# Optimization experiments

Hardware: AMD Instinct MI355X
Metric: run time of the kernel (lower is better)

## Reference

```python
import jax, jax.numpy as jnp
import numpy as np

M = 2          # n_mix
D_K = 128      # feature dim
TEMP = float(np.sqrt(D_K))  # temperature = d_k ** 0.5


def setup_inputs() -> dict:
    key = jax.random.key(0)
    k1, k2, k3, k4 = jax.random.split(key, 4)
    BS, N, N2 = 8, 2048, 2048
    qt = jax.random.normal(k1, (BS, N, D_K), jnp.float32)
    kt = jax.random.normal(k2, (BS, N2, D_K), jnp.float32)
    vt = jax.random.normal(k3, (BS, N2, D_K), jnp.float32)
    std = M ** -0.5
    kernel = jax.random.uniform(k4, (M, D_K), jnp.float32, -std, std)
    return {"qt": qt, "kt": kt, "vt": vt, "kernel": kernel}


def reference(qt, kt, vt, kernel):
    # channels_last path of MixtureOfSoftMaxACF.call, training=False (dropout = identity)
    BS, N, dk = qt.shape
    N2 = kt.shape[1]
    d = dk // M
    # mixture prior: softmax(kernel @ mean_q^T) over axis=1 (faithful to Softmax(axis=1))
    bar_qt = jnp.mean(qt, axis=1)                       # (BS, dk)
    prior_mix = jax.nn.softmax(kernel @ bar_qt.T, axis=1)  # (m, BS)
    prior_mix = prior_mix.reshape(BS * M, 1, 1)            # row-major reshape, as in TF
    # split features into mixtures via row-major reshape (as tf.reshape does)
    q = qt.reshape(BS * M, N, d)
    k = kt.reshape(BS * M, N2, d)
    att = jnp.einsum('bnd,bmd->bnm', q, k) / TEMP        # (BS*m, N, N2)
    att = jax.nn.softmax(att, axis=2)
    att = (att * prior_mix).reshape(BS, M, N, N2).sum(axis=1)  # (BS, N, N2)
    return att @ vt                                      # (BS, N, d_v)
```

## Files before the change

kernel.cpp:

```cpp
#include <hip/hip_runtime.h>
#include <hip/hip_fp16.h>

typedef float    f32x4 __attribute__((ext_vector_type(4)));
typedef _Float16 f16x2 __attribute__((ext_vector_type(2)));
typedef _Float16 f16x4 __attribute__((ext_vector_type(4)));
typedef _Float16 f16x8 __attribute__((ext_vector_type(8)));

#define BS 8
#define NN 2048
#define DK 128
#define DM 64
#define MIXOFF (1024 * DK)
#define QSCALE 0.12751744116926208f

#define MFMA32(a, b, c) __builtin_amdgcn_mfma_f32_16x16x32_f16((a), (b), (c), 0, 0, 0)
#define EXP2(x) __builtin_amdgcn_exp2f(x)

__device__ __forceinline__ f16x2 pkrtz(float x, float y) {
  return __builtin_bit_cast(f16x2, __builtin_amdgcn_cvt_pkrtz(x, y));
}

__device__ __forceinline__ void load_lds16(const _Float16* g, _Float16* l) {
  __builtin_amdgcn_global_load_lds(
      (const __attribute__((address_space(1))) void*)(uintptr_t)g,
      (__attribute__((address_space(3))) void*)(uint32_t)(uintptr_t)l, 16, 0, 0);
}

__global__ void prep_k(const float* __restrict__ kt, _Float16* __restrict__ kh,
                       const float* __restrict__ vt, _Float16* __restrict__ vT,
                       const float* __restrict__ qt, float* __restrict__ qpart) {
  __shared__ float tile[64][65];
  __shared__ float red[256];
  int blk = blockIdx.x;
  int t = threadIdx.x;
  if (blk < 512) {
    size_t base = (size_t)blk * 4096;
#pragma unroll
    for (int j = 0; j < 4; ++j) {
      size_t i = base + j * 1024 + t * 4;
      f32x4 v = *(const f32x4*)(kt + i);
      f16x4 h;
      h[0] = (_Float16)v[0]; h[1] = (_Float16)v[1];
      h[2] = (_Float16)v[2]; h[3] = (_Float16)v[3];
      *(f16x4*)(kh + i) = h;
    }
  } else if (blk < 1024) {
    int i2 = blk - 512;
    int b = i2 >> 6;
    int rem = i2 & 63;
    int j0 = (rem & 31) * 64;
    int c0 = (rem >> 5) * 64;
    int tx = t & 63, ty = t >> 6;
    const float* src = vt + ((size_t)b * NN + j0) * DK + c0;
#pragma unroll
    for (int rr = 0; rr < 16; ++rr) {
      int row = ty * 16 + rr;
      tile[row][tx] = src[(size_t)row * DK + tx];
    }
    __syncthreads();
    _Float16* dst = vT + ((size_t)b * DK + c0) * NN + j0;
    int chl = t >> 4;
    int k4 = (t & 15) * 4;
#pragma unroll
    for (int r2 = 0; r2 < 4; ++r2) {
      int ch = r2 * 16 + chl;
      f16x4 h;
      h[0] = (_Float16)tile[k4 + 0][ch]; h[1] = (_Float16)tile[k4 + 1][ch];
      h[2] = (_Float16)tile[k4 + 2][ch]; h[3] = (_Float16)tile[k4 + 3][ch];
      *(f16x4*)(dst + (size_t)ch * NN + k4) = h;
    }
  } else {
    int i = blk - 1024;
    int b = i >> 3, seg = i & 7;
    int c = t & 127, h = t >> 7;
    const float* p = qt + ((size_t)b * NN + seg * 256 + h * 128) * DK + c;
    float s = 0.f;
#pragma unroll 8
    for (int n = 0; n < 128; ++n) s += p[(size_t)n * DK];
    red[t] = s;
    __syncthreads();
    if (t < 128) qpart[(size_t)i * 128 + t] = red[t] + red[t + 128];
  }
}

#define STAGE(BUF, S) do {                                                \
    _Float16* db_ = stg + (BUF) * 16384;                                  \
    load_lds16(khg + gKst + (S) * 2048, db_ + t * 8);                     \
    load_lds16(vTg + gVst + (S) * 32, db_ + 4096 + t * 8);                \
    load_lds16(khg + gKst + 65536 + (S) * 2048, db_ + 8192 + t * 8);      \
    load_lds16(vTg + gVst + 1024 + (S) * 32, db_ + 12288 + t * 8);        \
  } while (0)

__global__ __launch_bounds__(512, 2) void attn_k(const float* __restrict__ qt,
                                                 const _Float16* __restrict__ khg,
                                                 const _Float16* __restrict__ vTg,
                                                 const float* __restrict__ kern,
                                                 const float* __restrict__ qpart,
                                                 float* __restrict__ out) {
  __shared__ __align__(16) char smem[65536];
  _Float16* stg = (_Float16*)smem;
  const int b = blockIdx.x & 7;
  const int qb = blockIdx.x >> 3;
  const int t = threadIdx.x;
  const int wv = t >> 6;
  const int m = wv >> 2;
  const int kh = (wv >> 1) & 1;
  const int u = wv & 1;
  const int lane = t & 63;
  const int quad = lane >> 4, l16 = lane & 15;
  const int perm = ((l16 >> 2) << 3) | (l16 & 3);
  const int bq = b * (NN * DK);
  const int bV = b * (DK * NN);

  f16x8 qf[2][2];
#pragma unroll
  for (int su = 0; su < 2; ++su)
#pragma unroll
    for (int c = 0; c < 2; ++c) {
      const float* qp_ = qt + bq + m * MIXOFF +
                         (qb * 64 + u * 32 + su * 16 + l16) * DM + quad * 8 + c * 32;
      f32x4 v0 = *(const f32x4*)qp_;
      f32x4 v1 = *(const f32x4*)(qp_ + 4);
      union { f16x8 v; f16x2 h[4]; } w;
      w.h[0] = pkrtz(v0[0] * QSCALE, v0[1] * QSCALE);
      w.h[1] = pkrtz(v0[2] * QSCALE, v0[3] * QSCALE);
      w.h[2] = pkrtz(v1[0] * QSCALE, v1[1] * QSCALE);
      w.h[3] = pkrtz(v1[2] * QSCALE, v1[3] * QSCALE);
      qf[su][c] = w.v;
    }

  const int mixu = t >> 8;
  const int qq8 = t & 255;
  const int rK = qq8 >> 3;
  const int uuK = (qq8 & 7) ^ ((rK & 3) ^ ((rK >> 3) << 1));
  const int chV = t >> 2;
  const int uuV = (t & 3) ^ ((chV + (chV >> 2)) & 3);
  const int gKst = bq + mixu * MIXOFF + rK * 64 + uuK * 8;
  const int gVst = bV + chV * NN + uuV * 8;

  const int gK = (l16 & 3) ^ ((l16 >> 2) << 1);
  const int hV = (l16 + (l16 >> 2)) & 3;
  const int kA = (quad ^ gK) * 8;
  const int kB = ((quad + 4) ^ gK) * 8;
  const int kr0 = m * 2048 + perm * 64;
  const int kr1 = m * 2048 + (perm + 4) * 64;
  const int vbase = 4096 + l16 * 32 + (quad ^ hV) * 8;
  const int khoff = kh * 8192;

  const f32x4 z = {0.f, 0.f, 0.f, 0.f};
  f32x4 acc[2][8];
  float lsum[2] = {0.f, 0.f};
#pragma unroll
  for (int su = 0; su < 2; ++su)
#pragma unroll
    for (int cc = 0; cc < 8; ++cc) acc[su][cc] = z;

  STAGE(0, 0);
  int buf = 0;
  for (int s = 0; s < 32; ++s) {
    __syncthreads();
    if (s + 1 < 32) STAGE(buf ^ 1, s + 1);
    const _Float16* sb_ = stg + buf * 16384 + khoff;
    f16x8 kf0 = *(const f16x8*)(sb_ + kr0 + kA);
    f16x8 kf1 = *(const f16x8*)(sb_ + kr0 + kB);
    f16x8 kf2 = *(const f16x8*)(sb_ + kr1 + kA);
    f16x8 kf3 = *(const f16x8*)(sb_ + kr1 + kB);
    f16x8 vf[8];
#pragma unroll
    for (int cc = 0; cc < 8; ++cc) vf[cc] = *(const f16x8*)(sb_ + vbase + cc * 512);
#pragma unroll
    for (int su = 0; su < 2; ++su) {
      f32x4 s0 = MFMA32(kf1, qf[su][1], MFMA32(kf0, qf[su][0], z));
      f32x4 s1 = MFMA32(kf3, qf[su][1], MFMA32(kf2, qf[su][0], z));
      float e0 = EXP2(s0[0]), e1 = EXP2(s0[1]), e2 = EXP2(s0[2]), e3 = EXP2(s0[3]);
      float e4 = EXP2(s1[0]), e5 = EXP2(s1[1]), e6 = EXP2(s1[2]), e7 = EXP2(s1[3]);
      lsum[su] += ((e0 + e1) + (e2 + e3)) + ((e4 + e5) + (e6 + e7));
      union { f16x8 v; f16x2 h[4]; } w;
      w.h[0] = pkrtz(e0, e1); w.h[1] = pkrtz(e2, e3);
      w.h[2] = pkrtz(e4, e5); w.h[3] = pkrtz(e6, e7);
#pragma unroll
      for (int cc = 0; cc < 8; ++cc) acc[su][cc] = MFMA32(vf[cc], w.v, acc[su][cc]);
    }
    buf ^= 1;
  }
  __syncthreads();

  float* obuf = (float*)smem;
  float* barL = (float*)(smem + 33792);
  float* lgp = (float*)(smem + 37888);
  float* exq = (float*)(smem + 37952);
  float* prp = (float*)(smem + 38016);
  float* lbuf = (float*)(smem + 38144);

#pragma unroll
  for (int su = 0; su < 2; ++su) {
    lsum[su] += __shfl_xor(lsum[su], 16);
    lsum[su] += __shfl_xor(lsum[su], 32);
  }
  for (int e = t; e < 1024; e += 512) {
    int bb = e >> 7, c = e & 127;
    float ss = 0.f;
#pragma unroll
    for (int seg = 0; seg < 8; ++seg) ss += qpart[(size_t)(bb * 8 + seg) * 128 + c];
    barL[e] = ss * (1.0f / 2048.0f);
  }
  if (kh == 0 && quad == 0)
#pragma unroll
    for (int su = 0; su < 2; ++su) lbuf[m * 64 + u * 32 + su * 16 + l16] = lsum[su];
  __syncthreads();
  if (kh == 1 && quad == 0)
#pragma unroll
    for (int su = 0; su < 2; ++su) lbuf[m * 64 + u * 32 + su * 16 + l16] += lsum[su];
  if (t < 16) {
    int mm = t >> 3, bb = t & 7;
    float ss = 0.f;
    for (int c = 0; c < DK; ++c) ss += kern[mm * DK + c] * barL[bb * 128 + c];
    lgp[t] = ss;
  }
  __syncthreads();
  if (t < 16) {
    int mm = t >> 3;
    float mx = lgp[mm * 8];
    for (int i = 1; i < 8; ++i) mx = fmaxf(mx, lgp[mm * 8 + i]);
    exq[t] = __expf(lgp[t] - mx);
  }
  __syncthreads();
  if (t < 16) {
    int mm = t >> 3;
    float sm = 0.f;
    for (int i = 0; i < 8; ++i) sm += exq[mm * 8 + i];
    prp[t] = exq[t] / sm;
  }
  __syncthreads();

  const float wm = prp[b * 2 + m];
  float rr[2];
#pragma unroll
  for (int su = 0; su < 2; ++su)
    rr[su] = wm / lbuf[m * 64 + u * 32 + su * 16 + l16];

  if (m == 0 && kh == 0) {
#pragma unroll
    for (int su = 0; su < 2; ++su) {
      int r_ = (u * 32 + su * 16 + l16) * 132 + quad * 4;
#pragma unroll
      for (int cc = 0; cc < 8; ++cc) *(f32x4*)&obuf[r_ + cc * 16] = acc[su][cc];
    }
  }
  __syncthreads();
  if (m == 0 && kh == 1) {
#pragma unroll
    for (int su = 0; su < 2; ++su) {
      int r_ = (u * 32 + su * 16 + l16) * 132 + quad * 4;
#pragma unroll
      for (int cc = 0; cc < 8; ++cc) {
        f32x4 o = *(const f32x4*)&obuf[r_ + cc * 16];
#pragma unroll
        for (int e = 0; e < 4; ++e) o[e] = (o[e] + acc[su][cc][e]) * rr[su];
        *(f32x4*)&obuf[r_ + cc * 16] = o;
      }
    }
  }
  __syncthreads();
  if (m == 1 && kh == 0) {
#pragma unroll
    for (int su = 0; su < 2; ++su) {
      int r_ = (u * 32 + su * 16 + l16) * 132 + quad * 4;
#pragma unroll
      for (int cc = 0; cc < 8; ++cc) {
        f32x4 o = *(const f32x4*)&obuf[r_ + cc * 16];
#pragma unroll
        for (int e = 0; e < 4; ++e) o[e] += acc[su][cc][e] * rr[su];
        *(f32x4*)&obuf[r_ + cc * 16] = o;
      }
    }
  }
  __syncthreads();
  if (m == 1 && kh == 1) {
#pragma unroll
    for (int su = 0; su < 2; ++su) {
      int r_ = (u * 32 + su * 16 + l16) * 132 + quad * 4;
#pragma unroll
      for (int cc = 0; cc < 8; ++cc) {
        f32x4 o = *(const f32x4*)&obuf[r_ + cc * 16];
#pragma unroll
        for (int e = 0; e < 4; ++e) o[e] += acc[su][cc][e] * rr[su];
        *(f32x4*)&obuf[r_ + cc * 16] = o;
      }
    }
  }
  __syncthreads();
  const int row = t >> 3;
  const int cb = (t & 7) * 16;
  float* op = out + ((size_t)b * NN + qb * 64 + row) * DK + cb;
#pragma unroll
  for (int g = 0; g < 4; ++g)
    *(f32x4*)(op + g * 4) = *(const f32x4*)&obuf[row * 132 + cb + g * 4];
}

extern "C" void kernel_launch(void* const* d_in, const int* in_sizes, int n_in,
                              void* d_out, int out_size, void* d_ws, size_t ws_size,
                              hipStream_t stream) {
  const float* qt = (const float*)d_in[0];
  const float* kt = (const float*)d_in[1];
  const float* vt = (const float*)d_in[2];
  const float* kern = (const float*)d_in[3];
  float* out = (float*)d_out;

  char* ws = (char*)d_ws;
  float* qpart = (float*)(ws + 4096);
  _Float16* khp = (_Float16*)(ws + 65536);
  _Float16* vTp = khp + (size_t)BS * NN * DK;

  prep_k<<<dim3(1088), dim3(256), 0, stream>>>(kt, khp, vt, vTp, qt, qpart);
  attn_k<<<dim3(256), dim3(512), 0, stream>>>(qt, khp, vTp, kern, qpart, out);
}
```

Baseline: 114.9 us.

## Widen attention tile to 64 keys per stage and reuse V fragments across queries

Each wave now covers all 64 query rows of the block (four 16-row sub-tiles), and the key dimension is split four ways across waves instead of two. Each stage loads 64 keys per mixture, so the loop runs 16 iterations instead of 32 and each V fragment read from LDS feeds four MFMAs. The K swizzle is adjusted to the new row layout. The epilogue now reduces four key-partial accumulators per mixture into two LDS output buffers, which are summed on store. The cost is 128 KB of LDS per block, which likely prevents two blocks per CU despite the launch bounds, plus more accumulator registers and more serialized epilogue phases.

```diff
diff --git a/kernel.cpp b/kernel.cpp
--- a/kernel.cpp
+++ b/kernel.cpp
@@ -83,12 +83,16 @@
   }
 }
 
-#define STAGE(BUF, S) do {                                                \
-    _Float16* db_ = stg + (BUF) * 16384;                                  \
-    load_lds16(khg + gKst + (S) * 2048, db_ + t * 8);                     \
-    load_lds16(vTg + gVst + (S) * 32, db_ + 4096 + t * 8);                \
-    load_lds16(khg + gKst + 65536 + (S) * 2048, db_ + 8192 + t * 8);      \
-    load_lds16(vTg + gVst + 1024 + (S) * 32, db_ + 12288 + t * 8);        \
+#define STAGE(BUF, S) do {                                                 \
+    _Float16* db_ = stg + (BUF) * 32768;                                   \
+    load_lds16(khg + gKst + (S) * 2048,          db_ + t * 8);             \
+    load_lds16(khg + gKst + 32768 + (S) * 2048,  db_ + 4096 + t * 8);      \
+    load_lds16(khg + gKst + 65536 + (S) * 2048,  db_ + 8192 + t * 8);      \
+    load_lds16(khg + gKst + 98304 + (S) * 2048,  db_ + 12288 + t * 8);     \
+    load_lds16(vTg + gVst + (S) * 32,            db_ + 16384 + t * 8);     \
+    load_lds16(vTg + gVst + 512 + (S) * 32,      db_ + 20480 + t * 8);     \
+    load_lds16(vTg + gVst + 1024 + (S) * 32,     db_ + 24576 + t * 8);     \
+    load_lds16(vTg + gVst + 1536 + (S) * 32,     db_ + 28672 + t * 8);     \
   } while (0)
 
 __global__ __launch_bounds__(512, 2) void attn_k(const float* __restrict__ qt,
@@ -97,28 +101,27 @@
                                                  const float* __restrict__ kern,
                                                  const float* __restrict__ qpart,
                                                  float* __restrict__ out) {
-  __shared__ __align__(16) char smem[65536];
+  __shared__ __align__(16) char smem[131072];
   _Float16* stg = (_Float16*)smem;
   const int b = blockIdx.x & 7;
   const int qb = blockIdx.x >> 3;
   const int t = threadIdx.x;
   const int wv = t >> 6;
   const int m = wv >> 2;
-  const int kh = (wv >> 1) & 1;
-  const int u = wv & 1;
+  const int kq = wv & 3;
   const int lane = t & 63;
   const int quad = lane >> 4, l16 = lane & 15;
   const int perm = ((l16 >> 2) << 3) | (l16 & 3);
   const int bq = b * (NN * DK);
   const int bV = b * (DK * NN);
 
-  f16x8 qf[2][2];
-#pragma unroll
-  for (int su = 0; su < 2; ++su)
+  f16x8 qf[4][2];
+#pragma unroll
+  for (int su = 0; su < 4; ++su)
 #pragma unroll
     for (int c = 0; c < 2; ++c) {
       const float* qp_ = qt + bq + m * MIXOFF +
-                         (qb * 64 + u * 32 + su * 16 + l16) * DM + quad * 8 + c * 32;
+                         (qb * 64 + su * 16 + l16) * DM + quad * 8 + c * 32;
       f32x4 v0 = *(const f32x4*)qp_;
       f32x4 v1 = *(const f32x4*)(qp_ + 4);
       union { f16x8 v; f16x2 h[4]; } w;
@@ -132,44 +135,41 @@
   const int mixu = t >> 8;
   const int qq8 = t & 255;
   const int rK = qq8 >> 3;
-  const int uuK = (qq8 & 7) ^ ((rK & 3) ^ ((rK >> 3) << 1));
+  const int uuK = (qq8 & 7) ^ ((rK & 3) ^ (((rK >> 3) & 1) << 2));
   const int chV = t >> 2;
   const int uuV = (t & 3) ^ ((chV + (chV >> 2)) & 3);
   const int gKst = bq + mixu * MIXOFF + rK * 64 + uuK * 8;
   const int gVst = bV + chV * NN + uuV * 8;
 
-  const int gK = (l16 & 3) ^ ((l16 >> 2) << 1);
+  const int gK = (l16 & 3) ^ (((l16 >> 2) & 1) << 2);
   const int hV = (l16 + (l16 >> 2)) & 3;
   const int kA = (quad ^ gK) * 8;
   const int kB = ((quad + 4) ^ gK) * 8;
-  const int kr0 = m * 2048 + perm * 64;
-  const int kr1 = m * 2048 + (perm + 4) * 64;
-  const int vbase = 4096 + l16 * 32 + (quad ^ hV) * 8;
-  const int khoff = kh * 8192;
+  const int kbase = kq * 4096 + m * 2048 + perm * 64;
+  const int vbase = 16384 + kq * 4096 + l16 * 32 + (quad ^ hV) * 8;
 
   const f32x4 z = {0.f, 0.f, 0.f, 0.f};
-  f32x4 acc[2][8];
-  float lsum[2] = {0.f, 0.f};
-#pragma unroll
-  for (int su = 0; su < 2; ++su)
+  f32x4 acc[4][8];
+  float lsum[4] = {0.f, 0.f, 0.f, 0.f};
+#pragma unroll
+  for (int su = 0; su < 4; ++su)
 #pragma unroll
     for (int cc = 0; cc < 8; ++cc) acc[su][cc] = z;
 
   STAGE(0, 0);
   int buf = 0;
-  for (int s = 0; s < 32; ++s) {
+  for (int s = 0; s < 16; ++s) {
     __syncthreads();
-    if (s + 1 < 32) STAGE(buf ^ 1, s + 1);
-    const _Float16* sb_ = stg + buf * 16384 + khoff;
-    f16x8 kf0 = *(const f16x8*)(sb_ + kr0 + kA);
-    f16x8 kf1 = *(const f16x8*)(sb_ + kr0 + kB);
-    f16x8 kf2 = *(const f16x8*)(sb_ + kr1 + kA);
-    f16x8 kf3 = *(const f16x8*)(sb_ + kr1 + kB);
-    f16x8 vf[8];
-#pragma unroll
-    for (int cc = 0; cc < 8; ++cc) vf[cc] = *(const f16x8*)(sb_ + vbase + cc * 512);
-#pragma unroll
-    for (int su = 0; su < 2; ++su) {
+    if (s + 1 < 16) STAGE(buf ^ 1, s + 1);
+    const _Float16* sb_ = stg + buf * 32768;
+    const _Float16* kb_ = sb_ + kbase;
+    f16x8 kf0 = *(const f16x8*)(kb_ + kA);
+    f16x8 kf1 = *(const f16x8*)(kb_ + kB);
+    f16x8 kf2 = *(const f16x8*)(kb_ + 256 + kA);
+    f16x8 kf3 = *(const f16x8*)(kb_ + 256 + kB);
+    f16x8 pw[4];
+#pragma unroll
+    for (int su = 0; su < 4; ++su) {
       f32x4 s0 = MFMA32(kf1, qf[su][1], MFMA32(kf0, qf[su][0], z));
       f32x4 s1 = MFMA32(kf3, qf[su][1], MFMA32(kf2, qf[su][0], z));
       float e0 = EXP2(s0[0]), e1 = EXP2(s0[1]), e2 = EXP2(s0[2]), e3 = EXP2(s0[3]);
@@ -178,22 +178,29 @@
       union { f16x8 v; f16x2 h[4]; } w;
       w.h[0] = pkrtz(e0, e1); w.h[1] = pkrtz(e2, e3);
       w.h[2] = pkrtz(e4, e5); w.h[3] = pkrtz(e6, e7);
-#pragma unroll
-      for (int cc = 0; cc < 8; ++cc) acc[su][cc] = MFMA32(vf[cc], w.v, acc[su][cc]);
+      pw[su] = w.v;
+    }
+    const _Float16* vb_ = sb_ + vbase;
+#pragma unroll
+    for (int cc = 0; cc < 8; ++cc) {
+      f16x8 vf = *(const f16x8*)(vb_ + cc * 512);
+#pragma unroll
+      for (int su = 0; su < 4; ++su) acc[su][cc] = MFMA32(vf, pw[su], acc[su][cc]);
     }
     buf ^= 1;
   }
   __syncthreads();
 
-  float* obuf = (float*)smem;
-  float* barL = (float*)(smem + 33792);
-  float* lgp = (float*)(smem + 37888);
-  float* exq = (float*)(smem + 37952);
-  float* prp = (float*)(smem + 38016);
-  float* lbuf = (float*)(smem + 38144);
-
-#pragma unroll
-  for (int su = 0; su < 2; ++su) {
+  float* obuf0 = (float*)smem;
+  float* obuf1 = (float*)(smem + 33792);
+  float* barL = (float*)(smem + 67584);
+  float* lgp = (float*)(smem + 71680);
+  float* exq = (float*)(smem + 71744);
+  float* prp = (float*)(smem + 71808);
+  float* lbuf = (float*)(smem + 71936);
+
+#pragma unroll
+  for (int su = 0; su < 4; ++su) {
     lsum[su] += __shfl_xor(lsum[su], 16);
     lsum[su] += __shfl_xor(lsum[su], 32);
   }
@@ -204,13 +211,10 @@
     for (int seg = 0; seg < 8; ++seg) ss += qpart[(size_t)(bb * 8 + seg) * 128 + c];
     barL[e] = ss * (1.0f / 2048.0f);
   }
-  if (kh == 0 && quad == 0)
-#pragma unroll
-    for (int su = 0; su < 2; ++su) lbuf[m * 64 + u * 32 + su * 16 + l16] = lsum[su];
-  __syncthreads();
-  if (kh == 1 && quad == 0)
-#pragma unroll
-    for (int su = 0; su < 2; ++su) lbuf[m * 64 + u * 32 + su * 16 + l16] += lsum[su];
+  if (quad == 0)
+#pragma unroll
+    for (int su = 0; su < 4; ++su) lbuf[wv * 64 + su * 16 + l16] = lsum[su];
+  __syncthreads();
   if (t < 16) {
     int mm = t >> 3, bb = t & 7;
     float ss = 0.f;
@@ -234,68 +238,57 @@
   __syncthreads();
 
   const float wm = prp[b * 2 + m];
-  float rr[2];
-#pragma unroll
-  for (int su = 0; su < 2; ++su)
-    rr[su] = wm / lbuf[m * 64 + u * 32 + su * 16 + l16];
-
-  if (m == 0 && kh == 0) {
-#pragma unroll
-    for (int su = 0; su < 2; ++su) {
-      int r_ = (u * 32 + su * 16 + l16) * 132 + quad * 4;
-#pragma unroll
-      for (int cc = 0; cc < 8; ++cc) *(f32x4*)&obuf[r_ + cc * 16] = acc[su][cc];
-    }
-  }
-  __syncthreads();
-  if (m == 0 && kh == 1) {
-#pragma unroll
-    for (int su = 0; su < 2; ++su) {
-      int r_ = (u * 32 + su * 16 + l16) * 132 + quad * 4;
+  float rr[4];
+#pragma unroll
+  for (int su = 0; su < 4; ++su) {
+    int q = su * 16 + l16;
+    rr[su] = wm / (((lbuf[(m * 4 + 0) * 64 + q] + lbuf[(m * 4 + 1) * 64 + q]) +
+                    (lbuf[(m * 4 + 2) * 64 + q] + lbuf[(m * 4 + 3) * 64 + q])));
+  }
+
+  float* ob = (m == 0) ? obuf0 : obuf1;
+  if (kq == 0) {
+#pragma unroll
+    for (int su = 0; su < 4; ++su) {
+      int r_ = (su * 16 + l16) * 132 + quad * 4;
 #pragma unroll
       for (int cc = 0; cc < 8; ++cc) {
-        f32x4 o = *(const f32x4*)&obuf[r_ + cc * 16];
-#pragma unroll
-        for (int e = 0; e < 4; ++e) o[e] = (o[e] + acc[su][cc][e]) * rr[su];
-        *(f32x4*)&obuf[r_ + cc * 16] = o;
+        f32x4 o;
+#pragma unroll
+        for (int e = 0; e < 4; ++e) o[e] = acc[su][cc][e] * rr[su];
+        *(f32x4*)&ob[r_ + cc * 16] = o;
       }
     }
   }
   __syncthreads();
-  if (m == 1 && kh == 0) {
-#pragma unroll
-    for (int su = 0; su < 2; ++su) {
-      int r_ = (u * 32 + su * 16 + l16) * 132 + quad * 4;
-#pragma unroll
-      for (int cc = 0; cc < 8; ++cc) {
-        f32x4 o = *(const f32x4*)&obuf[r_ + cc * 16];
-#pragma unroll
-        for (int e = 0; e < 4; ++e) o[e] += acc[su][cc][e] * rr[su];
-        *(f32x4*)&obuf[r_ + cc * 16] = o;
+  for (int ph = 1; ph < 4; ++ph) {
+    if (kq == ph) {
+#pragma unroll
+      for (int su = 0; su < 4; ++su) {
+        int r_ = (su * 16 + l16) * 132 + quad * 4;
+#pragma unroll
+        for (int cc = 0; cc < 8; ++cc) {
+          f32x4 o = *(const f32x4*)&ob[r_ + cc * 16];
+#pragma unroll
+          for (int e = 0; e < 4; ++e) o[e] += acc[su][cc][e] * rr[su];
+          *(f32x4*)&ob[r_ + cc * 16] = o;
+        }
       }
     }
-  }
-  __syncthreads();
-  if (m == 1 && kh == 1) {
-#pragma unroll
-    for (int su = 0; su < 2; ++su) {
-      int r_ = (u * 32 + su * 16 + l16) * 132 + quad * 4;
-#pragma unroll
-      for (int cc = 0; cc < 8; ++cc) {
-        f32x4 o = *(const f32x4*)&obuf[r_ + cc * 16];
-#pragma unroll
-        for (int e = 0; e < 4; ++e) o[e] += acc[su][cc][e] * rr[su];
-        *(f32x4*)&obuf[r_ + cc * 16] = o;
-      }
-    }
-  }
-  __syncthreads();
+    __syncthreads();
+  }
+
   const int row = t >> 3;
   const int cb = (t & 7) * 16;
   float* op = out + ((size_t)b * NN + qb * 64 + row) * DK + cb;
 #pragma unroll
-  for (int g = 0; g < 4; ++g)
-    *(f32x4*)(op + g * 4) = *(const f32x4*)&obuf[row * 132 + cb + g * 4];
+  for (int g = 0; g < 4; ++g) {
+    f32x4 a = *(const f32x4*)&obuf0[row * 132 + cb + g * 4];
+    f32x4 c = *(const f32x4*)&obuf1[row * 132 + cb + g * 4];
+#pragma unroll
+    for (int e = 0; e < 4; ++e) a[e] += c[e];
+    *(f32x4*)(op + g * 4) = a;
+  }
 }
 
 extern "C" void kernel_launch(void* const* d_in, const int* in_sizes, int n_in,
```

Result: slower. 119.2 us (+3.8%).
